# Kernel optimization log

Hardware: AMD Instinct MI355X
Metric: run time of the kernel (lower is better)

The kernel has to match this reference:

```python
import jax, jax.numpy as jnp
import numpy as np
import math

D = 1024  # output_dim (power of 2)
IN = 1024  # input dim
CAP = int(math.log2(D))  # number of butterfly stages


def _gen_indices(s):
    """Static FFT-butterfly index lists (numpy, computed at trace time)."""
    def ind_s(k):
        if k == 0:
            return [np.array([1, 0])]
        temp = np.arange(2 ** k)
        list0 = [np.concatenate([temp + 2 ** k, temp])]
        list1 = ind_s(k - 1)
        for i in range(k):
            list0.append(np.concatenate([list1[i], list1[i] + 2 ** k]))
        return list0

    t = ind_s(int(math.log2(s // 2)))
    cap = int(math.log2(s))
    ind_exe = [np.asarray(t[i], dtype=np.int32) for i in range(cap)]
    ind_param = []
    for i in range(cap):
        ind = np.concatenate([np.arange(0, s, 2 ** i) + j for j in range(2 ** i)]).astype(np.int32)
        ind_param.append(ind)
    return ind_exe, ind_param


IND_EXE, IND_PARAM = _gen_indices(D)


def setup_inputs() -> dict:
    key = jax.random.key(0)
    ks = jax.random.split(key, 9)
    B = 8192
    x = jax.random.normal(ks[0], (B, IN), dtype=jnp.float32)
    state = jax.random.normal(ks[1], (B, D), dtype=jnp.float32)
    theta = jax.random.uniform(ks[2], (CAP, D // 2), minval=-3.14, maxval=3.14, dtype=jnp.float32)
    U = jax.random.uniform(ks[3], (IN, 3 * D), minval=-0.01, maxval=0.01, dtype=jnp.float32)
    W_r = jax.random.uniform(ks[4], (D, D), minval=-0.01, maxval=0.01, dtype=jnp.float32)
    W_g = jax.random.uniform(ks[5], (D, D), minval=-0.01, maxval=0.01, dtype=jnp.float32)
    bias_r = jnp.full((D,), 2.0, dtype=jnp.float32)
    bias_g = jnp.zeros((D,), dtype=jnp.float32)
    bias_c = jnp.full((D,), 0.01, dtype=jnp.float32)
    return {"x": x, "state": state, "theta": theta, "U": U, "W_r": W_r,
            "W_g": W_g, "bias_r": bias_r, "bias_g": bias_g, "bias_c": bias_c}


def reference(x, state, theta, U, W_r, W_g, bias_r, bias_g, bias_c):
    # fft_param: rotation coefficients, permuted by the static ind_param lists
    cos_list = jnp.concatenate([jnp.cos(theta), jnp.cos(theta)], axis=1)   # [CAP, D]
    sin_list = jnp.concatenate([jnp.sin(theta), -jnp.sin(theta)], axis=1)  # [CAP, D]
    v1 = jnp.stack([cos_list[i][IND_PARAM[i]] for i in range(CAP)])  # [CAP, D]
    v2 = jnp.stack([sin_list[i][IND_PARAM[i]] for i in range(CAP)])  # [CAP, D]

    Ux = x @ U                                   # [B, 3D]
    U_cx, U_rx, U_gx = jnp.split(Ux, 3, axis=1)  # each [B, D]
    r = jax.nn.sigmoid(U_rx + state @ W_r + bias_r)
    g = jax.nn.sigmoid(U_gx + state @ W_g + bias_g)

    # butterfly orthogonal rotation of the state
    h = state
    for i in range(CAP):
        h = h * v1[i] + (h * v2[i])[:, IND_EXE[i]]

    # modReLU
    pre = r * h + U_cx
    c = jnp.sign(pre) * jax.nn.relu(jnp.abs(pre) + 0.001 + bias_c)

    out = g * state + (1.0 - g) * c
    return out
```

## Files before the change

kernel.cpp:

```cpp
#include <hip/hip_runtime.h>
#include <hip/hip_bf16.h>
#include <stdint.h>


typedef __bf16 bf16x8 __attribute__((ext_vector_type(8)));
typedef __bf16 bf16x4 __attribute__((ext_vector_type(4)));
typedef float f32x4 __attribute__((ext_vector_type(4)));

#define B_ROWS 8192

__device__ __forceinline__ void async16(__bf16* lds, const __hip_bfloat16* g) {
    __builtin_amdgcn_global_load_lds((const __attribute__((address_space(1))) void*)g,
                                     (__attribute__((address_space(3))) void*)lds,
                                     16, 0, 0);
}

__global__ __launch_bounds__(256) void prep_all(const float* __restrict__ x,
                                                const float* __restrict__ state,
                                                const float* __restrict__ theta,
                                                const float* __restrict__ U,
                                                const float* __restrict__ Wr,
                                                const float* __restrict__ Wg,
                                                __hip_bfloat16* __restrict__ xs,
                                                __hip_bfloat16* __restrict__ Wt0,
                                                __hip_bfloat16* __restrict__ Wt12,
                                                float* __restrict__ v1,
                                                float* __restrict__ v2) {
    __shared__ float tile[32][33];
    const int id = blockIdx.x;
    if (id < 8192) {
        const int row = id;
        const int col = threadIdx.x * 8;
        const float* src = (col < 1024) ? (x + (size_t)row * 1024 + col)
                                        : (state + (size_t)row * 1024 + (col - 1024));
        float4 a = *(const float4*)src;
        float4 b = *(const float4*)(src + 4);
        bf16x8 v;
        v[0] = (__bf16)a.x; v[1] = (__bf16)a.y; v[2] = (__bf16)a.z; v[3] = (__bf16)a.w;
        v[4] = (__bf16)b.x; v[5] = (__bf16)b.y; v[6] = (__bf16)b.z; v[7] = (__bf16)b.w;
        *(bf16x8*)((__bf16*)xs + (size_t)row * 2048 + col) = v;
    } else if (id < 13312) {
        const int wid = id - 8192;
        const float* src; int srcN, scol, sk;
        __hip_bfloat16* dst; int dstStride, dn, dk;
        if (wid < 1024) {
            int nx = wid & 31, ky = wid >> 5;
            src = U; srcN = 3072; scol = nx * 32; sk = ky * 32;
            dst = Wt0; dstStride = 1024; dn = nx * 32; dk = ky * 32;
        } else {
            int id2 = wid - 1024;
            int nx = id2 & 63, ky = id2 >> 6;
            int n0 = nx * 32, k0 = ky * 32;
            dst = Wt12; dstStride = 2048; dn = n0; dk = k0;
            if (k0 < 1024)      { src = U;  srcN = 3072; scol = 1024 + n0; sk = k0; }
            else if (n0 < 1024) { src = Wr; srcN = 1024; scol = n0;        sk = k0 - 1024; }
            else                { src = Wg; srcN = 1024; scol = n0 - 1024; sk = k0 - 1024; }
        }
        const int tx = threadIdx.x & 31, ty = threadIdx.x >> 5;
#pragma unroll
        for (int s = 0; s < 4; ++s)
            tile[ty + s * 8][tx] = src[(size_t)(sk + ty + s * 8) * srcN + scol + tx];
        __syncthreads();
#pragma unroll
        for (int s = 0; s < 4; ++s)
            dst[(size_t)(dn + ty + s * 8) * dstStride + dk + tx] = __float2bfloat16(tile[tx][ty + s * 8]);
    } else {
        int idx = (id - 13312) * 256 + threadIdx.x;
        int i = idx >> 10;
        int j = idx & 1023;
        int Q = 1024 >> i;
        int j0 = j / Q;
        int m = j & (Q - 1);
        int q = (m << i) + j0;
        float th = theta[i * 512 + (q & 511)];
        float c = cosf(th);
        float s = sinf(th);
        v1[idx] = c;
        v2[idx] = (q < 512) ? s : -s;
    }
}

template <int KEND, int BSTRIDE>
__device__ __forceinline__ void kloop(const __hip_bfloat16* __restrict__ A,
                                      const __hip_bfloat16* __restrict__ Bb,
                                      __bf16* As, __bf16* Bs, f32x4 acc[4][4],
                                      int t, int wm, int wn, int r0, int gq) {
    for (int k0 = 0; k0 < KEND; k0 += 32) {
#pragma unroll
        for (int p = 0; p < 2; ++p) {
            int c = p * 256 + t;
            int row = c >> 2;
            int jj = ((c & 3) ^ ((row >> 1) & 3)) * 8;
            async16(&As[c * 8], A + (size_t)row * 2048 + k0 + jj);
            async16(&Bs[c * 8], Bb + (size_t)row * BSTRIDE + k0 + jj);
        }
        __syncthreads();

        bf16x8 af[4], bf[4];
#pragma unroll
        for (int i = 0; i < 4; ++i) {
            int row = wm * 64 + i * 16 + r0;
            int cc = row * 4 + (gq ^ ((row >> 1) & 3));
            af[i] = *reinterpret_cast<const bf16x8*>(&As[cc * 8]);
        }
#pragma unroll
        for (int j = 0; j < 4; ++j) {
            int row = wn * 64 + j * 16 + r0;
            int cc = row * 4 + (gq ^ ((row >> 1) & 3));
            bf[j] = *reinterpret_cast<const bf16x8*>(&Bs[cc * 8]);
        }
#pragma unroll
        for (int i = 0; i < 4; ++i)
#pragma unroll
            for (int j = 0; j < 4; ++j)
                acc[i][j] = __builtin_amdgcn_mfma_f32_16x16x32_bf16(af[i], bf[j], acc[i][j], 0, 0, 0);
        __syncthreads();
    }
}

__global__ __launch_bounds__(256) void gemm_fused(const __hip_bfloat16* __restrict__ xs,
                                                  const __hip_bfloat16* __restrict__ Wt0,
                                                  const __hip_bfloat16* __restrict__ Wt12,
                                                  const float* __restrict__ bias_r,
                                                  const float* __restrict__ bias_g,
                                                  __hip_bfloat16* __restrict__ P) {
    __shared__ __align__(16) __bf16 As[128 * 32];
    __shared__ __align__(16) __bf16 Bs[128 * 32];

    const int nt = blockIdx.x;
    const int mt = blockIdx.y;
    const int group = nt >> 3;
    const int c0 = (nt & 7) * 128;
    const int mBase = mt * 128;

    const int t = threadIdx.x;
    const int lane = t & 63;
    const int wv = t >> 6;
    const int wm = wv & 1;
    const int wn = wv >> 1;
    const int r0 = lane & 15;
    const int gq = lane >> 4;

    f32x4 acc[4][4];
    const f32x4 zero = {0.f, 0.f, 0.f, 0.f};
#pragma unroll
    for (int i = 0; i < 4; ++i)
#pragma unroll
        for (int j = 0; j < 4; ++j) acc[i][j] = zero;

    const __hip_bfloat16* A = xs + (size_t)mBase * 2048;
    if (group == 0)
        kloop<1024, 1024>(A, Wt0 + (size_t)c0 * 1024, As, Bs, acc, t, wm, wn, r0, gq);
    else
        kloop<2048, 2048>(A, Wt12 + (size_t)((group == 2 ? 1024 : 0) + c0) * 2048,
                          As, Bs, acc, t, wm, wn, r0, gq);

#pragma unroll
    for (int i = 0; i < 4; ++i) {
#pragma unroll
        for (int j = 0; j < 4; ++j) {
#pragma unroll
            for (int reg = 0; reg < 4; ++reg) {
                int row = mBase + wm * 64 + i * 16 + gq * 4 + reg;
                int c = c0 + wn * 64 + j * 16 + r0;
                float v = acc[i][j][reg];
                if (group == 0) {
                    P[(size_t)row * 3072 + c] = __float2bfloat16(v);
                } else if (group == 1) {
                    float z = 1.0f / (1.0f + __expf(-(v + bias_r[c])));
                    P[(size_t)row * 3072 + 1024 + 2 * c] = __float2bfloat16(z);
                } else {
                    float z = 1.0f / (1.0f + __expf(-(v + bias_g[c])));
                    P[(size_t)row * 3072 + 1024 + 2 * c + 1] = __float2bfloat16(z);
                }
            }
        }
    }
}

__global__ __launch_bounds__(256) void fuse_kernel(const float* __restrict__ state,
                                                   const __hip_bfloat16* __restrict__ P,
                                                   const float* __restrict__ v1,
                                                   const float* __restrict__ v2,
                                                   const float* __restrict__ bias_c,
                                                   float* __restrict__ out) {
    __shared__ float hbuf[8][1024];
    const int t = threadIdx.x;
    const int rowBase = blockIdx.x * 8;

    float h[8][4];
    float sv[8][4];
#pragma unroll
    for (int r = 0; r < 8; ++r) {
        float4 s4 = ((const float4*)(state + (size_t)(rowBase + r) * 1024))[t];
        h[r][0] = s4.x; h[r][1] = s4.y; h[r][2] = s4.z; h[r][3] = s4.w;
        sv[r][0] = s4.x; sv[r][1] = s4.y; sv[r][2] = s4.z; sv[r][3] = s4.w;
        *(float4*)&hbuf[r][4 * t] = s4;
    }

    {
        __syncthreads();
        float4 w1 = *(const float4*)&v1[4 * t];
        float4 w2 = *(const float4*)&v2[4 * (t ^ 128)];
        const float w1v[4] = {w1.x, w1.y, w1.z, w1.w};
        const float w2v[4] = {w2.x, w2.y, w2.z, w2.w};
#pragma unroll
        for (int r = 0; r < 8; ++r) {
            float4 pr = *(const float4*)&hbuf[r][4 * (t ^ 128)];
            const float pv[4] = {pr.x, pr.y, pr.z, pr.w};
#pragma unroll
            for (int e = 0; e < 4; ++e) h[r][e] = h[r][e] * w1v[e] + pv[e] * w2v[e];
        }
        __syncthreads();
    }
    {
#pragma unroll
        for (int r = 0; r < 8; ++r)
            *(float4*)&hbuf[r][4 * t] = (float4){h[r][0], h[r][1], h[r][2], h[r][3]};
        __syncthreads();
        float4 w1 = *(const float4*)&v1[1024 + 4 * t];
        float4 w2 = *(const float4*)&v2[1024 + 4 * (t ^ 64)];
        const float w1v[4] = {w1.x, w1.y, w1.z, w1.w};
        const float w2v[4] = {w2.x, w2.y, w2.z, w2.w};
#pragma unroll
        for (int r = 0; r < 8; ++r) {
            float4 pr = *(const float4*)&hbuf[r][4 * (t ^ 64)];
            const float pv[4] = {pr.x, pr.y, pr.z, pr.w};
#pragma unroll
            for (int e = 0; e < 4; ++e) h[r][e] = h[r][e] * w1v[e] + pv[e] * w2v[e];
        }
    }
#pragma unroll
    for (int i = 2; i <= 7; ++i) {
        const int H = 512 >> i;
        const int lm = H >> 2;
        float4 w1 = *(const float4*)&v1[i * 1024 + 4 * t];
        float4 w2 = *(const float4*)&v2[i * 1024 + 4 * (t ^ lm)];
        const float w1v[4] = {w1.x, w1.y, w1.z, w1.w};
        const float w2v[4] = {w2.x, w2.y, w2.z, w2.w};
#pragma unroll
        for (int r = 0; r < 8; ++r) {
#pragma unroll
            for (int e = 0; e < 4; ++e) {
                float p = __shfl_xor(h[r][e], lm, 64);
                h[r][e] = h[r][e] * w1v[e] + p * w2v[e];
            }
        }
    }
    {
        float4 w1 = *(const float4*)&v1[8 * 1024 + 4 * t];
        float4 w2 = *(const float4*)&v2[8 * 1024 + 4 * t];
        const float w1v[4] = {w1.x, w1.y, w1.z, w1.w};
        const float w2v[4] = {w2.x, w2.y, w2.z, w2.w};
#pragma unroll
        for (int r = 0; r < 8; ++r) {
            float nh[4];
#pragma unroll
            for (int e = 0; e < 4; ++e) nh[e] = h[r][e] * w1v[e] + h[r][e ^ 2] * w2v[e ^ 2];
#pragma unroll
            for (int e = 0; e < 4; ++e) h[r][e] = nh[e];
        }
        float4 u1 = *(const float4*)&v1[9 * 1024 + 4 * t];
        float4 u2 = *(const float4*)&v2[9 * 1024 + 4 * t];
        const float u1v[4] = {u1.x, u1.y, u1.z, u1.w};
        const float u2v[4] = {u2.x, u2.y, u2.z, u2.w};
#pragma unroll
        for (int r = 0; r < 8; ++r) {
            float nh[4];
#pragma unroll
            for (int e = 0; e < 4; ++e) nh[e] = h[r][e] * u1v[e] + h[r][e ^ 1] * u2v[e ^ 1];
#pragma unroll
            for (int e = 0; e < 4; ++e) h[r][e] = nh[e];
        }
    }

    const float4 bc = ((const float4*)bias_c)[t];
    const float bcv[4] = {bc.x, bc.y, bc.z, bc.w};
#pragma unroll
    for (int r = 0; r < 8; ++r) {
        const int row = rowBase + r;
        const __hip_bfloat16* Pr = P + (size_t)row * 3072;
        bf16x4 ux = *(const bf16x4*)((const __bf16*)Pr + 4 * t);
        bf16x8 rg = *(const bf16x8*)((const __bf16*)Pr + 1024 + 8 * t);
        float o[4];
#pragma unroll
        for (int e = 0; e < 4; ++e) {
            float Ucx = (float)ux[e];
            float rr  = (float)rg[2 * e];
            float gg  = (float)rg[2 * e + 1];
            float pre = rr * h[r][e] + Ucx;
            float mag = fabsf(pre) + 0.001f + bcv[e];
            float c = (pre > 0.f) ? mag : ((pre < 0.f) ? -mag : 0.f);
            o[e] = gg * sv[r][e] + (1.f - gg) * c;
        }
        ((float4*)(out + (size_t)row * 1024))[t] = (float4){o[0], o[1], o[2], o[3]};
    }
}

extern "C" void kernel_launch(void* const* d_in, const int* in_sizes, int n_in,
                              void* d_out, int out_size, void* d_ws, size_t ws_size,
                              hipStream_t stream) {
    const float* x      = (const float*)d_in[0];
    const float* state  = (const float*)d_in[1];
    const float* theta  = (const float*)d_in[2];
    const float* U      = (const float*)d_in[3];
    const float* W_r    = (const float*)d_in[4];
    const float* W_g    = (const float*)d_in[5];
    const float* bias_r = (const float*)d_in[6];
    const float* bias_g = (const float*)d_in[7];
    const float* bias_c = (const float*)d_in[8];
    float* out = (float*)d_out;

    __hip_bfloat16* xs   = (__hip_bfloat16*)d_ws;
    __hip_bfloat16* Wt0  = xs + (size_t)B_ROWS * 2048;
    __hip_bfloat16* Wt12 = Wt0 + (size_t)1024 * 1024;
    __hip_bfloat16* P    = Wt12 + (size_t)2048 * 2048;
    float* v1 = (float*)(P + (size_t)B_ROWS * 3072);
    float* v2 = v1 + 10 * 1024;

    prep_all<<<13352, 256, 0, stream>>>(x, state, theta, U, W_r, W_g, xs, Wt0, Wt12, v1, v2);
    gemm_fused<<<dim3(24, 64), 256, 0, stream>>>(xs, Wt0, Wt12, bias_r, bias_g, P);
    fuse_kernel<<<1024, 256, 0, stream>>>(state, P, v1, v2, bias_c, out);
}
```

Baseline: 288.9 us.

## Compute r and g gate GEMM tiles in one block sharing the A tile

The r and g gate GEMMs now run in the same workgroup. Each A tile loaded into LDS feeds two B tiles, and the block keeps two accumulator sets. The sigmoid outputs are written as packed bf16 pairs, and the grid shrinks from 24 to 16 column tiles. This halves A-operand traffic for the gate GEMMs but doubles accumulator registers, which can lower occupancy, and makes the gate blocks twice as long, which may worsen load balance.

```diff
diff --git a/kernel.cpp b/kernel.cpp
--- a/kernel.cpp
+++ b/kernel.cpp
@@ -5,6 +5,7 @@
 
 typedef __bf16 bf16x8 __attribute__((ext_vector_type(8)));
 typedef __bf16 bf16x4 __attribute__((ext_vector_type(4)));
+typedef __bf16 bf16x2 __attribute__((ext_vector_type(2)));
 typedef float f32x4 __attribute__((ext_vector_type(4)));
 
 #define B_ROWS 8192
@@ -80,22 +81,21 @@
     }
 }
 
-template <int KEND, int BSTRIDE>
-__device__ __forceinline__ void kloop(const __hip_bfloat16* __restrict__ A,
-                                      const __hip_bfloat16* __restrict__ Bb,
-                                      __bf16* As, __bf16* Bs, f32x4 acc[4][4],
-                                      int t, int wm, int wn, int r0, int gq) {
-    for (int k0 = 0; k0 < KEND; k0 += 32) {
+
+__device__ __forceinline__ void kloop_c(const __hip_bfloat16* __restrict__ A,
+                                        const __hip_bfloat16* __restrict__ Bb,
+                                        __bf16* As, __bf16* Bs, f32x4 acc[4][4],
+                                        int t, int wm, int wn, int r0, int gq) {
+    for (int k0 = 0; k0 < 1024; k0 += 32) {
 #pragma unroll
         for (int p = 0; p < 2; ++p) {
             int c = p * 256 + t;
             int row = c >> 2;
             int jj = ((c & 3) ^ ((row >> 1) & 3)) * 8;
             async16(&As[c * 8], A + (size_t)row * 2048 + k0 + jj);
-            async16(&Bs[c * 8], Bb + (size_t)row * BSTRIDE + k0 + jj);
-        }
-        __syncthreads();
-
+            async16(&Bs[c * 8], Bb + (size_t)row * 1024 + k0 + jj);
+        }
+        __syncthreads();
         bf16x8 af[4], bf[4];
 #pragma unroll
         for (int i = 0; i < 4; ++i) {
@@ -114,6 +114,49 @@
 #pragma unroll
             for (int j = 0; j < 4; ++j)
                 acc[i][j] = __builtin_amdgcn_mfma_f32_16x16x32_bf16(af[i], bf[j], acc[i][j], 0, 0, 0);
+        __syncthreads();
+    }
+}
+
+__device__ __forceinline__ void kloop_rg(const __hip_bfloat16* __restrict__ A,
+                                         const __hip_bfloat16* __restrict__ B1,
+                                         const __hip_bfloat16* __restrict__ B2,
+                                         __bf16* As, __bf16* Bs1, __bf16* Bs2,
+                                         f32x4 accr[4][4], f32x4 accg[4][4],
+                                         int t, int wm, int wn, int r0, int gq) {
+    for (int k0 = 0; k0 < 2048; k0 += 32) {
+#pragma unroll
+        for (int p = 0; p < 2; ++p) {
+            int c = p * 256 + t;
+            int row = c >> 2;
+            int jj = ((c & 3) ^ ((row >> 1) & 3)) * 8;
+            size_t off = (size_t)row * 2048 + k0 + jj;
+            async16(&As[c * 8], A + off);
+            async16(&Bs1[c * 8], B1 + off);
+            async16(&Bs2[c * 8], B2 + off);
+        }
+        __syncthreads();
+        bf16x8 af[4], b1[4], b2[4];
+#pragma unroll
+        for (int i = 0; i < 4; ++i) {
+            int row = wm * 64 + i * 16 + r0;
+            int cc = row * 4 + (gq ^ ((row >> 1) & 3));
+            af[i] = *reinterpret_cast<const bf16x8*>(&As[cc * 8]);
+        }
+#pragma unroll
+        for (int j = 0; j < 4; ++j) {
+            int row = wn * 64 + j * 16 + r0;
+            int cc = row * 4 + (gq ^ ((row >> 1) & 3));
+            b1[j] = *reinterpret_cast<const bf16x8*>(&Bs1[cc * 8]);
+            b2[j] = *reinterpret_cast<const bf16x8*>(&Bs2[cc * 8]);
+        }
+#pragma unroll
+        for (int i = 0; i < 4; ++i)
+#pragma unroll
+            for (int j = 0; j < 4; ++j) {
+                accr[i][j] = __builtin_amdgcn_mfma_f32_16x16x32_bf16(af[i], b1[j], accr[i][j], 0, 0, 0);
+                accg[i][j] = __builtin_amdgcn_mfma_f32_16x16x32_bf16(af[i], b2[j], accg[i][j], 0, 0, 0);
+            }
         __syncthreads();
     }
 }
@@ -125,12 +168,11 @@
                                                   const float* __restrict__ bias_g,
                                                   __hip_bfloat16* __restrict__ P) {
     __shared__ __align__(16) __bf16 As[128 * 32];
-    __shared__ __align__(16) __bf16 Bs[128 * 32];
+    __shared__ __align__(16) __bf16 Bs1[128 * 32];
+    __shared__ __align__(16) __bf16 Bs2[128 * 32];
 
     const int nt = blockIdx.x;
     const int mt = blockIdx.y;
-    const int group = nt >> 3;
-    const int c0 = (nt & 7) * 128;
     const int mBase = mt * 128;
 
     const int t = threadIdx.x;
@@ -141,37 +183,57 @@
     const int r0 = lane & 15;
     const int gq = lane >> 4;
 
-    f32x4 acc[4][4];
-    const f32x4 zero = {0.f, 0.f, 0.f, 0.f};
-#pragma unroll
-    for (int i = 0; i < 4; ++i)
-#pragma unroll
-        for (int j = 0; j < 4; ++j) acc[i][j] = zero;
-
     const __hip_bfloat16* A = xs + (size_t)mBase * 2048;
-    if (group == 0)
-        kloop<1024, 1024>(A, Wt0 + (size_t)c0 * 1024, As, Bs, acc, t, wm, wn, r0, gq);
-    else
-        kloop<2048, 2048>(A, Wt12 + (size_t)((group == 2 ? 1024 : 0) + c0) * 2048,
-                          As, Bs, acc, t, wm, wn, r0, gq);
-
-#pragma unroll
-    for (int i = 0; i < 4; ++i) {
-#pragma unroll
-        for (int j = 0; j < 4; ++j) {
-#pragma unroll
-            for (int reg = 0; reg < 4; ++reg) {
-                int row = mBase + wm * 64 + i * 16 + gq * 4 + reg;
-                int c = c0 + wn * 64 + j * 16 + r0;
-                float v = acc[i][j][reg];
-                if (group == 0) {
-                    P[(size_t)row * 3072 + c] = __float2bfloat16(v);
-                } else if (group == 1) {
-                    float z = 1.0f / (1.0f + __expf(-(v + bias_r[c])));
-                    P[(size_t)row * 3072 + 1024 + 2 * c] = __float2bfloat16(z);
-                } else {
-                    float z = 1.0f / (1.0f + __expf(-(v + bias_g[c])));
-                    P[(size_t)row * 3072 + 1024 + 2 * c + 1] = __float2bfloat16(z);
+
+    if (nt < 8) {
+        const int c0 = nt * 128;
+        f32x4 accr[4][4], accg[4][4];
+        const f32x4 zero = {0.f, 0.f, 0.f, 0.f};
+#pragma unroll
+        for (int i = 0; i < 4; ++i)
+#pragma unroll
+            for (int j = 0; j < 4; ++j) { accr[i][j] = zero; accg[i][j] = zero; }
+
+        kloop_rg(A, Wt12 + (size_t)c0 * 2048, Wt12 + (size_t)(1024 + c0) * 2048,
+                 As, Bs1, Bs2, accr, accg, t, wm, wn, r0, gq);
+
+#pragma unroll
+        for (int i = 0; i < 4; ++i) {
+#pragma unroll
+            for (int j = 0; j < 4; ++j) {
+#pragma unroll
+                for (int reg = 0; reg < 4; ++reg) {
+                    int row = mBase + wm * 64 + i * 16 + gq * 4 + reg;
+                    int c = c0 + wn * 64 + j * 16 + r0;
+                    float zr = 1.0f / (1.0f + __expf(-(accr[i][j][reg] + bias_r[c])));
+                    float zg = 1.0f / (1.0f + __expf(-(accg[i][j][reg] + bias_g[c])));
+                    bf16x2 pk;
+                    pk[0] = (__bf16)zr;
+                    pk[1] = (__bf16)zg;
+                    *(bf16x2*)((__bf16*)P + (size_t)row * 3072 + 1024 + 2 * c) = pk;
+                }
+            }
+        }
+    } else {
+        const int c0 = (nt - 8) * 128;
+        f32x4 acc[4][4];
+        const f32x4 zero = {0.f, 0.f, 0.f, 0.f};
+#pragma unroll
+        for (int i = 0; i < 4; ++i)
+#pragma unroll
+            for (int j = 0; j < 4; ++j) acc[i][j] = zero;
+
+        kloop_c(A, Wt0 + (size_t)c0 * 1024, As, Bs1, acc, t, wm, wn, r0, gq);
+
+#pragma unroll
+        for (int i = 0; i < 4; ++i) {
+#pragma unroll
+            for (int j = 0; j < 4; ++j) {
+#pragma unroll
+                for (int reg = 0; reg < 4; ++reg) {
+                    int row = mBase + wm * 64 + i * 16 + gq * 4 + reg;
+                    int c = c0 + wn * 64 + j * 16 + r0;
+                    P[(size_t)row * 3072 + c] = __float2bfloat16(acc[i][j][reg]);
                 }
             }
         }
@@ -319,6 +381,6 @@
     float* v2 = v1 + 10 * 1024;
 
     prep_all<<<13352, 256, 0, stream>>>(x, state, theta, U, W_r, W_g, xs, Wt0, Wt12, v1, v2);
-    gemm_fused<<<dim3(24, 64), 256, 0, stream>>>(xs, Wt0, Wt12, bias_r, bias_g, P);
+    gemm_fused<<<dim3(16, 64), 256, 0, stream>>>(xs, Wt0, Wt12, bias_r, bias_g, P);
     fuse_kernel<<<1024, 256, 0, stream>>>(state, P, v1, v2, bias_c, out);
 }
```

New measurement: 410.0 us. 1.42x slower.
